# Kernel tuning notes

Hardware: AMD Instinct MI355X
Metric: run time of the kernel (lower is better)

## Reference

```python
import jax, jax.numpy as jnp
import numpy as np

B, HQ, HK, S, D, HID, BS = 2, 32, 8, 8192, 128, 128, 16
NB = S // BS  # 512 pooled blocks


def rotate_half(x):
    h = x.shape[-1] // 2
    return jnp.concatenate([-x[..., h:], x[..., :h]], axis=-1)


def pool_cat(x):
    # avg + max pooling over block_size along the sequence dim, concat on feature dim
    b, h, s, d = x.shape
    xb = x.reshape(b, h, s // BS, BS, d)
    return jnp.concatenate([xb.mean(axis=3), xb.max(axis=3)], axis=-1)  # [b,h,NB,2d]


def setup_inputs() -> dict:
    key = jax.random.key(0)
    k0, k1, k2, k3 = jax.random.split(key, 4)
    q = jax.random.normal(k0, (B, HQ, S, D), jnp.float32)
    k = jax.random.normal(k1, (B, HK, S, D), jnp.float32)
    wq = jax.random.normal(k2, (HQ, 2 * D, HID), jnp.float32) / np.float32(np.sqrt(2 * D))
    wk = jax.random.normal(k3, (HK, 2 * D, HID), jnp.float32) / np.float32(np.sqrt(2 * D))
    # causal block mask
    mask = jnp.broadcast_to(jnp.tril(jnp.ones((NB, NB), bool))[None, None], (B, 1, NB, NB))
    # RoPE tables over pooled positions
    pos = jnp.arange(NB, dtype=jnp.float32)
    inv_freq = 1.0 / (10000.0 ** (jnp.arange(0, HID, 2, dtype=jnp.float32) / HID))
    freqs = pos[:, None] * inv_freq[None, :]              # [NB, HID/2]
    emb = jnp.concatenate([freqs, freqs], axis=-1)        # [NB, HID]
    cos = jnp.broadcast_to(jnp.cos(emb)[None], (B, NB, HID))
    sin = jnp.broadcast_to(jnp.sin(emb)[None], (B, NB, HID))
    return {"q": q, "k": k, "attention_mask": mask, "cos": cos, "sin": sin, "wq": wq, "wk": wk}


def reference(q, k, attention_mask, cos, sin, wq, wk):
    # pooled multi-head linear projections
    qh = jnp.einsum('bhnc,hcd->bhnd', pool_cat(q), wq)   # [B,HQ,NB,HID]
    kh = jnp.einsum('bhnc,hcd->bhnd', pool_cat(k), wk)   # [B,HK,NB,HID]
    # RoPE (unsqueeze_dim=1)
    c, s = cos[:, None], sin[:, None]
    qh = qh * c + rotate_half(qh) * s
    kh = kh * c + rotate_half(kh) * s
    # GQA: repeat kv heads
    kh = jnp.repeat(kh, HQ // HK, axis=1)                # [B,HQ,NB,HID]
    attn = jnp.einsum('bhqd,bhkd->bhqk', qh, kh) / jnp.sqrt(jnp.float32(HID))
    attn = jnp.where(attention_mask, attn, jnp.float32(-1e9))
    return jax.nn.softmax(attn, axis=-1)
```

## Files before the change

kernel.cpp:

```cpp
#include <hip/hip_runtime.h>

namespace {
constexpr int BB  = 2;
constexpr int HQ  = 32;
constexpr int HK  = 8;
constexpr int S   = 8192;
constexpr int D   = 128;
constexpr int HID = 128;
constexpr int BS  = 16;
constexpr int NB  = 512;
constexpr int C2D = 256;
constexpr int WTR = 512;
constexpr int BLK = 4096;
}

typedef __attribute__((ext_vector_type(8))) short short8;
typedef __attribute__((ext_vector_type(4))) float f32x4;

__device__ inline unsigned short f2bf(float f) {
  unsigned u = __builtin_bit_cast(unsigned, f);
  unsigned r = u + 0x7fff + ((u >> 16) & 1);
  return (unsigned short)(r >> 16);
}
__device__ inline float bf2f(unsigned short s) {
  unsigned u = ((unsigned)s) << 16;
  return __builtin_bit_cast(float, u);
}

__global__ __launch_bounds__(256) void wprep_kernel(
    const float* __restrict__ wq, const float* __restrict__ wk,
    unsigned short* __restrict__ wT)
{
  __shared__ float ts[32 * 33];
  const int t  = threadIdx.x;
  const int kc = blockIdx.x;
  const int hy = blockIdx.y;
  const float* w = (hy < HQ) ? (wq + (size_t)hy * C2D * HID)
                             : (wk + (size_t)(hy - HQ) * C2D * HID);
  for (int nc = 0; nc < 4; ++nc) {
    __syncthreads();
    {
      const int r = t >> 3, c4 = t & 7;
      *(float4*)&ts[r * 33 + 4 * c4] =
          *(const float4*)(w + (size_t)(kc * 32 + r) * HID + nc * 32 + 4 * c4);
    }
    __syncthreads();
    {
      const int n = t >> 3, g = t & 7;
      const int cb = 8 * (g & 3);
      short8 v;
#pragma unroll
      for (int j = 0; j < 8; ++j) {
        const float f = ts[(cb + j) * 33 + n];
        const unsigned short h = f2bf(f);
        v[j] = (short)((g < 4) ? h : f2bf(f - bf2f(h)));
      }
      unsigned short* dst = wT + ((size_t)hy * HID + nc * 32 + n) * WTR +
                            ((g < 4) ? 0 : 256) + kc * 32 + cb;
      *(short8*)dst = v;
    }
  }
}

__global__ __launch_bounds__(256) void pool_gemm_rope_kernel(
    const float* __restrict__ qx, const float* __restrict__ kx,
    const unsigned short* __restrict__ wT,
    const float* __restrict__ cosp, const float* __restrict__ sinp,
    unsigned short* __restrict__ qhb, unsigned short* __restrict__ khb)
{
  constexpr int AST = 520;
  constexpr int CST = 132;
  __shared__ unsigned short As[32 * AST];
  float* Cs = (float*)As;

  const int t  = threadIdx.x;
  const int n0 = blockIdx.x * 32;
  const int hy = blockIdx.y;
  const int b  = blockIdx.z;

  const float* x; unsigned short* o; int H; int h; bool isq;
  if (hy < HQ) { x = qx; o = qhb; H = HQ; h = hy; isq = true; }
  else         { x = kx; o = khb; H = HK; h = hy - HQ; isq = false; }

  const float* xb = x + (((size_t)b * H + h) * S + (size_t)n0 * BS) * D;
  for (int it = t; it < 32 * 32; it += 256) {
    const int m = it >> 5, d4 = it & 31;
    const float4* p = (const float4*)(xb + (size_t)m * BS * D) + d4;
    float4 v = p[0];
    float sx = v.x, sy = v.y, sz = v.z, sw = v.w;
    float mx = v.x, my = v.y, mz = v.z, mw = v.w;
#pragma unroll
    for (int i = 1; i < BS; ++i) {
      v = p[i * (D / 4)];
      sx += v.x; sy += v.y; sz += v.z; sw += v.w;
      mx = fmaxf(mx, v.x); my = fmaxf(my, v.y);
      mz = fmaxf(mz, v.z); mw = fmaxf(mw, v.w);
    }
    const float inv16 = 1.0f / 16.0f;
    float mn[4] = {sx * inv16, sy * inv16, sz * inv16, sw * inv16};
    float mv[4] = {mx, my, mz, mw};
    ushort4 mh, ml, xh, xl;
    mh.x = f2bf(mn[0]); ml.x = f2bf(mn[0] - bf2f(mh.x));
    mh.y = f2bf(mn[1]); ml.y = f2bf(mn[1] - bf2f(mh.y));
    mh.z = f2bf(mn[2]); ml.z = f2bf(mn[2] - bf2f(mh.z));
    mh.w = f2bf(mn[3]); ml.w = f2bf(mn[3] - bf2f(mh.w));
    xh.x = f2bf(mv[0]); xl.x = f2bf(mv[0] - bf2f(xh.x));
    xh.y = f2bf(mv[1]); xl.y = f2bf(mv[1] - bf2f(xh.y));
    xh.z = f2bf(mv[2]); xl.z = f2bf(mv[2] - bf2f(xh.z));
    xh.w = f2bf(mv[3]); xl.w = f2bf(mv[3] - bf2f(xh.w));
    unsigned short* row = &As[m * AST];
    *(ushort4*)(row + 4 * d4)       = mh;
    *(ushort4*)(row + 256 + 4 * d4) = ml;
    *(ushort4*)(row + 128 + 4 * d4) = xh;
    *(ushort4*)(row + 384 + 4 * d4) = xl;
  }
  __syncthreads();

  const int w    = t >> 6;
  const int lane = t & 63;
  const int col  = lane & 15;
  const int quad = lane >> 4;
  const int mtile = w & 1;
  const int nbase = (w >> 1) * 64;

  const unsigned short* arow = &As[(size_t)(mtile * 16 + col) * AST + quad * 8];
  const unsigned short* bp = wT + ((size_t)hy * HID + nbase + col) * WTR + quad * 8;

  f32x4 acc[4];
#pragma unroll
  for (int i = 0; i < 4; ++i) acc[i] = (f32x4){0.f, 0.f, 0.f, 0.f};

#pragma unroll
  for (int ks = 0; ks < 8; ++ks) {
    const short8 ahi = *(const short8*)(arow + ks * 32);
    const short8 alo = *(const short8*)(arow + 256 + ks * 32);
#pragma unroll
    for (int nt = 0; nt < 4; ++nt) {
      const short8 bhi = *(const short8*)(bp + (size_t)nt * 16 * WTR + ks * 32);
      const short8 blo = *(const short8*)(bp + (size_t)nt * 16 * WTR + 256 + ks * 32);
      acc[nt] = __builtin_amdgcn_mfma_f32_16x16x32_bf16(ahi, bhi, acc[nt], 0, 0, 0);
      acc[nt] = __builtin_amdgcn_mfma_f32_16x16x32_bf16(ahi, blo, acc[nt], 0, 0, 0);
      acc[nt] = __builtin_amdgcn_mfma_f32_16x16x32_bf16(alo, bhi, acc[nt], 0, 0, 0);
    }
  }
  __syncthreads();

#pragma unroll
  for (int nt = 0; nt < 4; ++nt)
#pragma unroll
    for (int r = 0; r < 4; ++r)
      Cs[(size_t)(mtile * 16 + quad * 4 + r) * CST + nbase + nt * 16 + col] =
          acc[nt][r];
  __syncthreads();

  const int dt = t & 31, mt = t >> 5;
  const int d0 = dt * 4, m0 = mt * 4;
  const float sgn = (d0 < 64) ? -1.0f : 1.0f;
  const float qscale = isq ? 0.08838834764831843f : 1.0f;
  float4 ov[4];
#pragma unroll
  for (int i = 0; i < 4; ++i) {
    const int n = n0 + m0 + i;
    const float4 cv = *(const float4*)(cosp + ((size_t)b * NB + n) * HID + d0);
    const float4 sv = *(const float4*)(sinp + ((size_t)b * NB + n) * HID + d0);
    const float4 cur = *(const float4*)&Cs[(m0 + i) * CST + d0];
    const float4 pr  = *(const float4*)&Cs[(m0 + i) * CST + (d0 ^ 64)];
    ov[i].x = (cur.x * cv.x + sgn * pr.x * sv.x) * qscale;
    ov[i].y = (cur.y * cv.y + sgn * pr.y * sv.y) * qscale;
    ov[i].z = (cur.z * cv.z + sgn * pr.z * sv.z) * qscale;
    ov[i].w = (cur.w * cv.w + sgn * pr.w * sv.w) * qscale;
  }
  __syncthreads();
#pragma unroll
  for (int i = 0; i < 4; ++i)
    *(float4*)&Cs[(m0 + i) * CST + d0] = ov[i];
  __syncthreads();

  unsigned short* obase = o + ((size_t)b * H + h) * (size_t)(32 * BLK) +
                          (size_t)(n0 >> 4) * BLK;
#pragma unroll
  for (int j = 0; j < 4; ++j) {
    const int c = t + 256 * j;
    const int k16c = c >> 9;
    const int fi   = (c >> 6) & 7;
    const int ln   = c & 63;
    const int colr = ln & 15, quadr = ln >> 4;
    const int n = k16c * 16 + colr;
    const int dstart = (fi & 3) * 32 + quadr * 8;
    const float* src = &Cs[n * CST + dstart];
    short8 outv;
    if (fi < 4) {
#pragma unroll
      for (int e = 0; e < 8; ++e) outv[e] = (short)f2bf(src[e]);
    } else {
#pragma unroll
      for (int e = 0; e < 8; ++e) {
        const float f = src[e];
        outv[e] = (short)f2bf(f - bf2f(f2bf(f)));
      }
    }
    *(short8*)(obase + (size_t)k16c * BLK + (fi * 64 + ln) * 8) = outv;
  }
}

__global__ __launch_bounds__(256) void attn_kernel(
    const unsigned short* __restrict__ qhb,
    const unsigned short* __restrict__ khb,
    float* __restrict__ out)
{
  __shared__ float rs_lds[16];

  const int t = threadIdx.x;
  const int w = t >> 6;
  const int lane = t & 63;
  const int col = lane & 15;
  const int quad = lane >> 4;
  const int strip = blockIdx.x;
  const int h = blockIdx.y;
  const int b = blockIdx.z;

  const unsigned short* qfb = qhb + (((size_t)b * HQ + h) * 32 + strip) * BLK;
  const unsigned short* kfb = khb + (((size_t)b * HK + (h >> 2)) * 32) * BLK;
  float* obase = out + (((size_t)b * HQ + h) * NB) * (size_t)NB;

  if (t < 16) rs_lds[t] = 0.f;
  __syncthreads();

  short8 qf[8];
#pragma unroll
  for (int fi = 0; fi < 8; ++fi)
    qf[fi] = *(const short8*)(qfb + (fi * 64 + lane) * 8);

  const int n = (w <= strip) ? ((strip - w) >> 2) + 1 : 0;

  f32x4 pbuf[8];
  float rs[4] = {0.f, 0.f, 0.f, 0.f};

#pragma unroll
  for (int ti = 0; ti < 8; ++ti) {
    if (ti < n) {
      const int k16 = w + 4 * ti;
      const unsigned short* kp = kfb + (size_t)k16 * BLK + lane * 8;
      short8 kf[8];
#pragma unroll
      for (int fi = 0; fi < 8; ++fi)
        kf[fi] = *(const short8*)(kp + fi * 512);
      f32x4 accA = {0.f, 0.f, 0.f, 0.f};
      f32x4 accB = {0.f, 0.f, 0.f, 0.f};
      f32x4 accC = {0.f, 0.f, 0.f, 0.f};
#pragma unroll
      for (int f = 0; f < 4; ++f) {
        accA = __builtin_amdgcn_mfma_f32_16x16x32_bf16(qf[f],     kf[f],     accA, 0, 0, 0);
        accB = __builtin_amdgcn_mfma_f32_16x16x32_bf16(qf[f],     kf[4 + f], accB, 0, 0, 0);
        accC = __builtin_amdgcn_mfma_f32_16x16x32_bf16(qf[4 + f], kf[f],     accC, 0, 0, 0);
      }
      const bool diag = (k16 == strip);
      f32x4 p;
#pragma unroll
      for (int r = 0; r < 4; ++r) {
        float v = __expf(accA[r] + accB[r] + accC[r]);
        if (diag && col > quad * 4 + r) v = 0.f;
        p[r] = v;
        rs[r] += v;
      }
      pbuf[ti] = p;
    }
  }

#pragma unroll
  for (int r = 0; r < 4; ++r) {
    float v = rs[r];
    v += __shfl_xor(v, 1, 64);
    v += __shfl_xor(v, 2, 64);
    v += __shfl_xor(v, 4, 64);
    v += __shfl_xor(v, 8, 64);
    if (col == 0) atomicAdd(&rs_lds[quad * 4 + r], v);
  }

  {
    const int r = t >> 4;
    const float4 z = make_float4(0.f, 0.f, 0.f, 0.f);
    for (int c4 = (strip + 1) * 4 + (t & 15); c4 < 128; c4 += 16)
      *(float4*)(obase + (size_t)(strip * 16 + r) * NB + 4 * c4) = z;
  }

  __syncthreads();

  float inv[4];
#pragma unroll
  for (int r = 0; r < 4; ++r) inv[r] = 1.0f / rs_lds[quad * 4 + r];

#pragma unroll
  for (int ti = 0; ti < 8; ++ti) {
    if (ti < n) {
      const int k16 = w + 4 * ti;
#pragma unroll
      for (int r = 0; r < 4; ++r)
        obase[(size_t)(strip * 16 + quad * 4 + r) * NB + k16 * 16 + col] =
            pbuf[ti][r] * inv[r];
    }
  }
}

extern "C" void kernel_launch(void* const* d_in, const int* in_sizes, int n_in,
                              void* d_out, int out_size, void* d_ws, size_t ws_size,
                              hipStream_t stream)
{
  const float* q    = (const float*)d_in[0];
  const float* k    = (const float*)d_in[1];
  const float* cosp = (const float*)d_in[3];
  const float* sinp = (const float*)d_in[4];
  const float* wq   = (const float*)d_in[5];
  const float* wk   = (const float*)d_in[6];
  float* out = (float*)d_out;

  unsigned short* qhb = (unsigned short*)d_ws;
  unsigned short* khb = qhb + (size_t)BB * HQ * 32 * BLK;
  unsigned short* wTp = khb + (size_t)BB * HK * 32 * BLK;

  hipLaunchKernelGGL(wprep_kernel, dim3(8, HQ + HK), dim3(256),
                     0, stream, wq, wk, wTp);
  hipLaunchKernelGGL(pool_gemm_rope_kernel, dim3(NB / 32, HQ + HK, BB), dim3(256),
                     0, stream, q, k, wTp, cosp, sinp, qhb, khb);
  hipLaunchKernelGGL(attn_kernel, dim3(32, HQ, BB), dim3(256),
                     0, stream, qhb, khb, out);
}
```

Baseline: 470.4 us.

## Stage softmax probabilities in LDS and write output rows with coalesced nontemporal stores

The attention kernel now writes each exp value into a shared-memory tile covering a full 16x512 row strip, which is zero-initialised up front. After the row sums are reduced, it writes the whole strip to global memory as contiguous float4 nontemporal stores. Before, it used scattered per-element stores plus a separate zero-fill loop. The pooling kernel also switches its streaming q/k reads to nontemporal loads. The change adds about 33 KB of LDS per block, which may reduce occupancy, plus extra syncs and LDS traffic, in exchange for fully coalesced output writes.

```diff
diff --git a/kernel.cpp b/kernel.cpp
--- a/kernel.cpp
+++ b/kernel.cpp
@@ -85,13 +85,13 @@
   const float* xb = x + (((size_t)b * H + h) * S + (size_t)n0 * BS) * D;
   for (int it = t; it < 32 * 32; it += 256) {
     const int m = it >> 5, d4 = it & 31;
-    const float4* p = (const float4*)(xb + (size_t)m * BS * D) + d4;
-    float4 v = p[0];
+    const f32x4* p = (const f32x4*)(xb + (size_t)m * BS * D) + d4;
+    f32x4 v = __builtin_nontemporal_load(p);
     float sx = v.x, sy = v.y, sz = v.z, sw = v.w;
     float mx = v.x, my = v.y, mz = v.z, mw = v.w;
 #pragma unroll
     for (int i = 1; i < BS; ++i) {
-      v = p[i * (D / 4)];
+      v = __builtin_nontemporal_load(p + i * (D / 4));
       sx += v.x; sy += v.y; sz += v.z; sw += v.w;
       mx = fmaxf(mx, v.x); my = fmaxf(my, v.y);
       mz = fmaxf(mz, v.z); mw = fmaxf(mw, v.w);
@@ -208,6 +208,8 @@
     const unsigned short* __restrict__ khb,
     float* __restrict__ out)
 {
+  constexpr int PST = 516;
+  __shared__ float Ps[16 * PST];
   __shared__ float rs_lds[16];
 
   const int t = threadIdx.x;
@@ -221,9 +223,18 @@
 
   const unsigned short* qfb = qhb + (((size_t)b * HQ + h) * 32 + strip) * BLK;
   const unsigned short* kfb = khb + (((size_t)b * HK + (h >> 2)) * 32) * BLK;
-  float* obase = out + (((size_t)b * HQ + h) * NB) * (size_t)NB;
+  float* obase = out + (((size_t)b * HQ + h) * NB + (size_t)strip * 16) * NB;
 
   if (t < 16) rs_lds[t] = 0.f;
+  {
+    const f32x4 z = {0.f, 0.f, 0.f, 0.f};
+#pragma unroll
+    for (int j = 0; j < 8; ++j) {
+      const int c = t + 256 * j;
+      const int row = c >> 7, c4 = c & 127;
+      *(f32x4*)&Ps[row * PST + 4 * c4] = z;
+    }
+  }
   __syncthreads();
 
   short8 qf[8];
@@ -233,7 +244,6 @@
 
   const int n = (w <= strip) ? ((strip - w) >> 2) + 1 : 0;
 
-  f32x4 pbuf[8];
   float rs[4] = {0.f, 0.f, 0.f, 0.f};
 
 #pragma unroll
@@ -255,15 +265,13 @@
         accC = __builtin_amdgcn_mfma_f32_16x16x32_bf16(qf[4 + f], kf[f],     accC, 0, 0, 0);
       }
       const bool diag = (k16 == strip);
-      f32x4 p;
 #pragma unroll
       for (int r = 0; r < 4; ++r) {
         float v = __expf(accA[r] + accB[r] + accC[r]);
         if (diag && col > quad * 4 + r) v = 0.f;
-        p[r] = v;
+        Ps[(quad * 4 + r) * PST + k16 * 16 + col] = v;
         rs[r] += v;
       }
-      pbuf[ti] = p;
     }
   }
 
@@ -276,29 +284,18 @@
     v += __shfl_xor(v, 8, 64);
     if (col == 0) atomicAdd(&rs_lds[quad * 4 + r], v);
   }
-
-  {
-    const int r = t >> 4;
-    const float4 z = make_float4(0.f, 0.f, 0.f, 0.f);
-    for (int c4 = (strip + 1) * 4 + (t & 15); c4 < 128; c4 += 16)
-      *(float4*)(obase + (size_t)(strip * 16 + r) * NB + 4 * c4) = z;
-  }
-
-  __syncthreads();
-
-  float inv[4];
-#pragma unroll
-  for (int r = 0; r < 4; ++r) inv[r] = 1.0f / rs_lds[quad * 4 + r];
-
-#pragma unroll
-  for (int ti = 0; ti < 8; ++ti) {
-    if (ti < n) {
-      const int k16 = w + 4 * ti;
-#pragma unroll
-      for (int r = 0; r < 4; ++r)
-        obase[(size_t)(strip * 16 + quad * 4 + r) * NB + k16 * 16 + col] =
-            pbuf[ti][r] * inv[r];
-    }
+  __syncthreads();
+
+  if (t < 16) rs_lds[t] = 1.0f / rs_lds[t];
+  __syncthreads();
+
+#pragma unroll
+  for (int j = 0; j < 8; ++j) {
+    const int c = t + 256 * j;
+    const int row = c >> 7, c4 = c & 127;
+    f32x4 v = *(const f32x4*)&Ps[row * PST + 4 * c4];
+    v *= rs_lds[row];
+    __builtin_nontemporal_store(v, (f32x4*)(obase + (size_t)row * NB + 4 * c4));
   }
 }
 
```

Result: faster. 452.0 us (-3.9%).
